# Kernel tuning notes

Measured on AMD Instinct MI355X. Metric: run time of the kernel, lower is better.

The kernel has to match this reference:

```python
import jax, jax.numpy as jnp
import numpy as np

D_MODEL = 512
N_HEADS = 8
DH = D_MODEL // N_HEADS            # 64
Q_PROJ = D_MODEL // 2              # 256
KV_PROJ = (2 * D_MODEL) // 3       # 341
ROPE_DIM = D_MODEL // 8            # 64 total rope dims
R = ROPE_DIM // N_HEADS            # 8 rope dims per head
THETA = 10000.0
EPS = 1e-5
B, S = 2, 2048


def layernorm(x, g, b):
    m = jnp.mean(x, axis=-1, keepdims=True)
    v = jnp.var(x, axis=-1, keepdims=True)
    return (x - m) * jax.lax.rsqrt(v + EPS) * g + b


def rope_cos_sin(seq_len, dtype):
    inv_freq = THETA ** (-jnp.arange(0, R, 2, dtype=jnp.float32) / R)   # (R/2,)
    ang = jnp.arange(seq_len, dtype=jnp.float32)[:, None] * inv_freq   # (S, R/2)
    cos = jnp.concatenate([jnp.cos(ang), jnp.cos(ang)], axis=-1)        # (S, R)
    sin = jnp.concatenate([jnp.sin(ang), jnp.sin(ang)], axis=-1)
    return cos.astype(dtype), sin.astype(dtype)


def apply_rope(x, cos, sin):
    # x: (B, H, S, R); neox-style half rotation
    x1, x2 = jnp.split(x, 2, axis=-1)
    rot = jnp.concatenate([-x2, x1], axis=-1)
    return x * cos + rot * sin


def setup_inputs() -> dict:
    key = jax.random.key(0)
    ks = jax.random.split(key, 9)
    p = lambda k, shape: 0.01 * jax.random.normal(k, shape, jnp.float32)
    return {
        "x": jax.random.normal(ks[0], (B, S, D_MODEL), jnp.float32),
        "W_dq": p(ks[1], (D_MODEL, Q_PROJ)),
        "W_uq": p(ks[2], (Q_PROJ, D_MODEL)),
        "W_qr": p(ks[3], (Q_PROJ, ROPE_DIM)),
        "W_dkv": p(ks[4], (D_MODEL, KV_PROJ)),
        "W_ukv": p(ks[5], (KV_PROJ, 2 * D_MODEL)),
        "W_kr": p(ks[6], (D_MODEL, ROPE_DIM)),
        "W_o": p(ks[7], (D_MODEL, D_MODEL)),
        "q_ln_g": jnp.ones((Q_PROJ,), jnp.float32),
        "q_ln_b": jnp.zeros((Q_PROJ,), jnp.float32),
        "kv_ln_g": jnp.ones((KV_PROJ,), jnp.float32),
        "kv_ln_b": jnp.zeros((KV_PROJ,), jnp.float32),
    }


def reference(x, W_dq, W_uq, W_qr, W_dkv, W_ukv, W_kr, W_o,
              q_ln_g, q_ln_b, kv_ln_g, kv_ln_b):
    b, s, d = x.shape
    # --- low-rank Q path ---
    cq = layernorm(x @ W_dq, q_ln_g, q_ln_b)                      # (B,S,Q_PROJ)
    Q = (cq @ W_uq).reshape(b, s, N_HEADS, DH).transpose(0, 2, 1, 3)
    Qr = (cq @ W_qr).reshape(b, s, N_HEADS, R).transpose(0, 2, 1, 3)
    cos, sin = rope_cos_sin(s, x.dtype)
    Qr = apply_rope(Qr, cos, sin)
    q = jnp.concatenate([Q, Qr], axis=-1)                          # (B,H,S,DH+R)
    # --- low-rank KV path ---
    ckv = layernorm(x @ W_dkv, kv_ln_g, kv_ln_b)                  # (B,S,KV_PROJ)
    KV = ckv @ W_ukv                                              # (B,S,2*D)
    K, V = KV[..., :D_MODEL], KV[..., D_MODEL:]
    K = K.reshape(b, s, N_HEADS, DH).transpose(0, 2, 1, 3)
    Kr = (x @ W_kr).reshape(b, s, N_HEADS, R).transpose(0, 2, 1, 3)
    Kr = apply_rope(Kr, cos, sin)
    k = jnp.concatenate([K, Kr], axis=-1)                          # (B,H,S,DH+R)
    v = V.reshape(b, s, N_HEADS, DH).transpose(0, 2, 1, 3)         # (B,H,S,DH)
    # --- causal SDPA ---
    scale = 1.0 / jnp.sqrt(jnp.asarray(DH + R, x.dtype))
    scores = jnp.einsum('bhqd,bhkd->bhqk', q, k) * scale           # (B,H,S,S)
    mask = jnp.tril(jnp.ones((s, s), dtype=bool))
    scores = jnp.where(mask, scores, jnp.finfo(scores.dtype).min)
    attn = jax.nn.softmax(scores, axis=-1)
    out = jnp.einsum('bhqk,bhkd->bhqd', attn, v)
    out = out.transpose(0, 2, 1, 3).reshape(b, s, d)
    return out @ W_o.T, ckv
```

## Files before the change

kernel.cpp:

```cpp
#include <hip/hip_runtime.h>
#include <hip/hip_bf16.h>

#define BATCH 2
#define SEQ 2048
#define DM 512
#define NH 8
#define DHD 64
#define QP 256
#define KVP 341
#define DQKPAD 96
#define MROWS 4096

#define OFF_X     0
#define OFF_WO    2932224
#define OFF_QG    3194368
#define OFF_QB    3194624
#define OFF_KG    3194880
#define OFF_KB    3195221

#define T_DQ   0
#define T_DKV  131072
#define T_KR   327680
#define T_UQ   360448
#define T_QR   491520
#define T_UKV  507904
#define T_TOT  901120

#define NW_X   2097152
#define NW_WO  262144
#define NW_PAR 1194

#define G_X   262144
#define G_WO  32768
#define G_PAR 150
#define G_WT  112640
#define G_TOT (G_X + G_WO + G_PAR + G_WT)

#define NSPLIT 4

typedef __bf16 bf16x8 __attribute__((ext_vector_type(8)));
typedef float f32x4 __attribute__((ext_vector_type(4)));
typedef __hip_bfloat16 bf16;
typedef unsigned short u16;

static __device__ __forceinline__ bf16x8 ld_bf8(const bf16* p) {
    return __builtin_bit_cast(bf16x8, *(const uint4*)p);
}

#define GL16(gp, lp) __builtin_amdgcn_global_load_lds( \
    (const __attribute__((address_space(1))) void*)(gp), \
    (__attribute__((address_space(3))) void*)(lp), 16, 0, 0)

__global__ __launch_bounds__(256) void prep(
    const void* px, const void* pwdq, const void* pwuq, const void* pwqr,
    const void* pwdkv, const void* pwukv, const void* pwkr, const void* pwo,
    const void* pqg, const void* pqb, const void* pkg, const void* pkb,
    u16* __restrict__ arena, u16* __restrict__ WT, int* __restrict__ flagp)
{
    __shared__ int cnt;
    if (threadIdx.x == 0) cnt = 0;
    __syncthreads();
    int bad = 0;
    const u16* xs = (const u16*)px;
    for (int i = threadIdx.x; i < 2048; i += 256) {
        u16 u = xs[i];
        int e = (u >> 7) & 0xFF;
        if (u != 0 && (e < 90 || e > 164)) bad++;
    }
    #pragma unroll
    for (int m2 = 1; m2 < 64; m2 <<= 1) bad += __shfl_xor(bad, m2);
    if ((threadIdx.x & 63) == 0) atomicAdd(&cnt, bad);
    __syncthreads();
    const int f = (cnt > 256) ? 1 : 0;
    if (blockIdx.x == 0 && threadIdx.x == 0) *flagp = f;

    int gid = blockIdx.x * 256 + threadIdx.x;
    if (gid >= G_TOT) return;

    auto rdu = [&](const void* s, int i) -> u16 {
        if (f) return __builtin_bit_cast(u16, __float2bfloat16(((const float*)s)[i]));
        return ((const u16*)s)[i];
    };

    if (gid < G_X + G_WO) {
        const void* src = (gid < G_X) ? px : pwo;
        int base = (gid < G_X) ? OFF_X : OFF_WO;
        int i = (gid < G_X) ? gid : gid - G_X;
        u16 out[8];
        if (f) {
            const float* s = (const float*)src + i * 8;
            #pragma unroll
            for (int j = 0; j < 8; ++j) out[j] = __builtin_bit_cast(u16, __float2bfloat16(s[j]));
        } else {
            *(uint4*)out = ((const uint4*)src)[i];
        }
        *(uint4*)&arena[base + i * 8] = *(uint4*)out;
    } else if (gid < G_X + G_WO + G_PAR) {
        int i0 = (gid - G_X - G_WO) * 8;
        for (int j = 0; j < 8; ++j) {
            int i = i0 + j;
            if (i >= NW_PAR) break;
            if (i < 256)      arena[OFF_QG + i]         = rdu(pqg, i);
            else if (i < 512) arena[OFF_QB + (i - 256)] = rdu(pqb, i - 256);
            else if (i < 853) arena[OFF_KG + (i - 512)] = rdu(pkg, i - 512);
            else              arena[OFF_KB + (i - 853)] = rdu(pkb, i - 853);
        }
    } else {
        int loc = (gid - (G_X + G_WO + G_PAR)) * 8;
        const void* src; int n, k0, sN, klim, nok;
        if (loc < T_DKV)      { int l = loc;          n = l >> 9; k0 = l & 511; src = pwdq;  sN = 256;  klim = 512; nok = 1; }
        else if (loc < T_KR)  { int l = loc - T_DKV;  n = l >> 9; k0 = l & 511; src = pwdkv; sN = 341;  klim = 512; nok = (n < 341); }
        else if (loc < T_UQ)  { int l = loc - T_KR;   n = l >> 9; k0 = l & 511; src = pwkr;  sN = 64;   klim = 512; nok = 1; }
        else if (loc < T_QR)  { int l = loc - T_UQ;   n = l >> 8; k0 = l & 255; src = pwuq;  sN = 512;  klim = 256; nok = 1; }
        else if (loc < T_UKV) { int l = loc - T_QR;   n = l >> 8; k0 = l & 255; src = pwqr;  sN = 64;   klim = 256; nok = 1; }
        else                  { int l = loc - T_UKV;  n = l / 384; k0 = l % 384; src = pwukv; sN = 1024; klim = 341; nok = 1; }
        u16 out[8];
        #pragma unroll
        for (int j = 0; j < 8; ++j) {
            int k = k0 + j;
            out[j] = (nok && k < klim) ? rdu(src, k * sN + n) : (u16)0;
        }
        *(uint4*)&WT[loc] = *(uint4*)out;
    }
}

static __device__ __forceinline__ void rope_epi(
    f32x4 (&acc)[2][4], bf16* __restrict__ dst, int m0, int w, int g, int lr, int tid, bool scaleq)
{
    const float SCv = 0.11785113019775793f;
    #pragma unroll
    for (int mt = 0; mt < 2; ++mt)
    #pragma unroll
    for (int r = 0; r < 4; ++r) {
        int gm = m0 + w * 32 + mt * 16 + g * 4 + r;
        int s = gm & 2047, b = gm >> 11;
        float ang = (float)s * exp2f(-(float)(lr & 3) * 3.3219280948873623f);
        float sn, cs;
        sincosf(ang, &sn, &cs);
        #pragma unroll
        for (int nt = 0; nt < 4; ++nt) {
            float v = acc[mt][nt][r];
            float pt = __shfl_xor(v, 4);
            float o = (lr & 4) ? fmaf(pt, sn, v * cs) : fmaf(-pt, sn, v * cs);
            if (scaleq) o *= SCv;
            int h = (nt * 16 + lr) >> 3, j = lr & 7;
            dst[((size_t)(b * NH + h) * SEQ + s) * DQKPAD + 64 + j] = __float2bfloat16(o);
        }
    }
    for (int u = tid; u < 128 * 96; u += 256) {
        int rw = u / 96, rem = u - rw * 96;
        int h = rem / 12, c = rem - h * 12;
        int row = m0 + rw, b2 = row >> 11, s2 = row & 2047;
        *(unsigned int*)&dst[((size_t)(b2 * NH + h) * SEQ + s2) * DQKPAD + 72 + c * 2] = 0u;
    }
}

static __device__ __forceinline__ void gemm_body(
    int bx, int by,
    const bf16* __restrict__ A, int lda,
    const bf16* __restrict__ BT, int ldb,
    int N, int Kpad, int mode,
    void* __restrict__ C0, int ldc,
    bf16* __restrict__ kv_k, bf16* __restrict__ kv_v,
    const int* __restrict__ flagp, float* __restrict__ C0f,
    bf16* LB)
{
    bf16* Al = LB;
    bf16* Bl = LB + 128 * 64;
    const int tid = threadIdx.x;
    const int m0 = by * 128, n0 = bx * 64;
    const int lane = tid & 63, w = tid >> 6;
    const int g = lane >> 4, lr = lane & 15;
    f32x4 acc[2][4] = {};
    const int r8 = lane >> 3;
    const int xr8 = ((lane & 7) ^ r8) * 8;
    const int swx = (lr & 7) << 4;

    for (int k0 = 0; k0 < Kpad; k0 += 64) {
        #pragma unroll
        for (int i = 0; i < 4; ++i)
            GL16(&A[(size_t)(m0 + w * 32 + i * 8 + r8) * lda + k0 + xr8],
                 (char*)Al + w * 4096 + i * 1024);
        #pragma unroll
        for (int i = 0; i < 2; ++i)
            GL16(&BT[(size_t)(n0 + w * 16 + i * 8 + r8) * ldb + k0 + xr8],
                 (char*)Bl + w * 2048 + i * 1024);
        __syncthreads();
        #pragma unroll
        for (int ks = 0; ks < 2; ++ks) {
            const int cs = (ks * 64 + g * 16) ^ swx;
            bf16x8 a0 = ld_bf8((const bf16*)((const char*)Al + (w * 32 + lr) * 128 + cs));
            bf16x8 a1 = ld_bf8((const bf16*)((const char*)Al + (w * 32 + 16 + lr) * 128 + cs));
            #pragma unroll
            for (int nt = 0; nt < 4; ++nt) {
                bf16x8 b = ld_bf8((const bf16*)((const char*)Bl + (nt * 16 + lr) * 128 + cs));
                acc[0][nt] = __builtin_amdgcn_mfma_f32_16x16x32_bf16(a0, b, acc[0][nt], 0, 0, 0);
                acc[1][nt] = __builtin_amdgcn_mfma_f32_16x16x32_bf16(a1, b, acc[1][nt], 0, 0, 0);
            }
        }
        __syncthreads();
    }

    if (mode == 0 && n0 == 640) {
        rope_epi(acc, kv_k, m0, w, g, lr, tid, false);
        return;
    }
    if (mode == 4 && n0 == DM) {
        rope_epi(acc, (bf16*)C0, m0, w, g, lr, tid, true);
        return;
    }
    if (mode == 3 && n0 >= DM) {
        const int h = (n0 - DM) >> 6;
        const int b = m0 >> 11, s0 = m0 & 2047;
        bf16* T = LB;
        #pragma unroll
        for (int mt = 0; mt < 2; ++mt)
        #pragma unroll
        for (int nt = 0; nt < 4; ++nt)
        #pragma unroll
        for (int r = 0; r < 4; ++r) {
            int dv = nt * 16 + lr;
            int sl = w * 32 + mt * 16 + g * 4 + r;
            T[dv * 136 + sl] = __float2bfloat16(acc[mt][nt][r]);
        }
        __syncthreads();
        const int row = tid >> 2, coff = (tid & 3) * 32;
        bf16* dst = &kv_v[((size_t)(b * NH + h) * DHD + row) * SEQ + s0 + coff];
        const bf16* srcp = &T[row * 136 + coff];
        #pragma unroll
        for (int q2 = 0; q2 < 4; ++q2)
            *(uint4*)(dst + q2 * 8) = *(const uint4*)(srcp + q2 * 8);
        return;
    }

    const float SCv = 0.11785113019775793f;
    const int f32o = (mode == 1 && flagp) ? *flagp : 0;
    #pragma unroll
    for (int mt = 0; mt < 2; ++mt)
    #pragma unroll
    for (int nt = 0; nt < 4; ++nt)
    #pragma unroll
    for (int r = 0; r < 4; ++r) {
        int gm = m0 + w * 32 + mt * 16 + g * 4 + r;
        int gn = n0 + nt * 16 + lr;
        float v = acc[mt][nt][r];
        if (mode == 0) {
            ((bf16*)C0)[(size_t)gm * ldc + gn] = __float2bfloat16(v);
        } else if (mode == 1) {
            if (f32o) C0f[(size_t)gm * ldc + gn] = v;
            else ((bf16*)C0)[(size_t)gm * ldc + gn] = __float2bfloat16(v);
        } else if (mode == 4) {
            int b = gm >> 11, s = gm & 2047;
            int h = gn >> 6, dh = gn & 63;
            ((bf16*)C0)[((size_t)(b * NH + h) * SEQ + s) * DQKPAD + dh] = __float2bfloat16(v * SCv);
        } else {
            int b = gm >> 11, s = gm & 2047;
            int h = gn >> 6, dh = gn & 63;
            kv_k[((size_t)(b * NH + h) * SEQ + s) * DQKPAD + dh] = __float2bfloat16(v);
        }
    }
}

__global__ __launch_bounds__(256) void gemm128(
    const bf16* __restrict__ A, int lda,
    const bf16* __restrict__ BT, int ldb,
    int N, int Kpad, int mode,
    void* __restrict__ C0, int ldc,
    bf16* __restrict__ kv_k, bf16* __restrict__ kv_v,
    const int* __restrict__ flagp, float* __restrict__ C0f)
{
    __shared__ __align__(16) bf16 LB[128 * 64 + 64 * 64];
    gemm_body(blockIdx.x, blockIdx.y, A, lda, BT, ldb, N, Kpad, mode,
              C0, ldc, kv_k, kv_v, flagp, C0f, LB);
}

__global__ __launch_bounds__(256) void gemm_dual(
    const bf16* __restrict__ A1, const bf16* __restrict__ BT1, void* __restrict__ C1,
    const bf16* __restrict__ A2, const bf16* __restrict__ BT2,
    bf16* __restrict__ kv_k, bf16* __restrict__ kv_v)
{
    __shared__ __align__(16) bf16 LB[128 * 64 + 64 * 64];
    if (blockIdx.x < 9) {
        gemm_body(blockIdx.x, blockIdx.y, A1, QP, BT1, QP, 576, QP, 4,
                  C1, 0, nullptr, nullptr, nullptr, nullptr, LB);
    } else {
        gemm_body(blockIdx.x - 9, blockIdx.y, A2, 384, BT2, 384, 1024, 384, 3,
                  nullptr, 0, kv_k, kv_v, nullptr, nullptr, LB);
    }
}

__global__ __launch_bounds__(256) void ln_both(
    const bf16* __restrict__ y,
    const bf16* __restrict__ qg, const bf16* __restrict__ qb,
    const bf16* __restrict__ kg, const bf16* __restrict__ kb,
    bf16* __restrict__ cq, bf16* __restrict__ ckv_b, float* __restrict__ ckv_f,
    bf16* __restrict__ ckvp, const int* __restrict__ flagp)
{
    const int w = threadIdx.x >> 6, lane = threadIdx.x & 63;
    const int blk = blockIdx.x;
    if (blk < 1024) {
        const int row = blk * 4 + w;
        const bf16* yr = y + (size_t)row * 704;
        float s = 0.f, ss = 0.f;
        for (int i = lane; i < 256; i += 64) { float v = __bfloat162float(yr[i]); s += v; ss += v * v; }
        #pragma unroll
        for (int m = 1; m < 64; m <<= 1) { s += __shfl_xor(s, m); ss += __shfl_xor(ss, m); }
        float mean = s * (1.f / 256.f);
        float var = ss * (1.f / 256.f) - mean * mean;
        float rstd = rsqrtf(var + 1e-5f);
        for (int i = lane; i < 256; i += 64) {
            float v = (__bfloat162float(yr[i]) - mean) * rstd * __bfloat162float(qg[i]) + __bfloat162float(qb[i]);
            cq[(size_t)row * 256 + i] = __float2bfloat16(v);
        }
    } else {
        const int row = (blk - 1024) * 4 + w;
        const bf16* yr = y + (size_t)row * 704 + 256;
        const int f32o = *flagp;
        float s = 0.f, ss = 0.f;
        for (int i = lane; i < KVP; i += 64) { float v = __bfloat162float(yr[i]); s += v; ss += v * v; }
        #pragma unroll
        for (int m = 1; m < 64; m <<= 1) { s += __shfl_xor(s, m); ss += __shfl_xor(ss, m); }
        float mean = s * (1.f / 341.f);
        float var = ss * (1.f / 341.f) - mean * mean;
        float rstd = rsqrtf(var + 1e-5f);
        for (int i = lane; i < KVP; i += 64) {
            float v = (__bfloat162float(yr[i]) - mean) * rstd * __bfloat162float(kg[i]) + __bfloat162float(kb[i]);
            if (f32o) ckv_f[(size_t)row * KVP + i] = v;
            else ckv_b[(size_t)row * KVP + i] = __float2bfloat16(v);
            ckvp[(size_t)row * 384 + i] = __float2bfloat16(v);
        }
        for (int i = KVP + lane; i < 384; i += 64) ckvp[(size_t)row * 384 + i] = __float2bfloat16(0.f);
    }
}

__global__ __launch_bounds__(256) void attn_split3(
    const bf16* __restrict__ qa, const bf16* __restrict__ ka, const bf16* __restrict__ vat,
    bf16* __restrict__ po, float* __restrict__ mlm, float* __restrict__ mll)
{
    __shared__ __align__(16) bf16 Kl[64][128];
    __shared__ __align__(16) bf16 Vt[64][72];
    __shared__ __align__(16) bf16 Pl[4][16][72];
    const int sp = blockIdx.x, pr = blockIdx.y, bh = blockIdx.z;
    const int tid = threadIdx.x, w = tid >> 6, lane = tid & 63;
    const int g = lane >> 4, lr = lane & 15;
    const size_t base = (size_t)bh * SEQ;
    const float L2E = 1.4426950408889634f;
    const bf16* vb = vat + (size_t)bh * DHD * SEQ;

    uint4 kreg0, kreg1, kreg2, vreg0, vreg1;
    const int vd = tid >> 2, vko = (tid & 3) * 16;
    const int kr0 = tid / 12,          ks0 = tid % 12;
    const int kr1 = (tid + 256) / 12,  ks1 = (tid + 256) % 12;
    const int kr2 = (tid + 512) / 12,  ks2 = (tid + 512) % 12;
    const int kx0 = (ks0 ^ (kr0 & 15)) * 8;
    const int kx1 = (ks1 ^ (kr1 & 15)) * 8;
    const int kx2 = (ks2 ^ (kr2 & 15)) * 8;

    #define ISSUE_KV(j0)  do { \
        kreg0 = *(const uint4*)&ka[(base + (j0) + kr0) * DQKPAD + ks0 * 8]; \
        kreg1 = *(const uint4*)&ka[(base + (j0) + kr1) * DQKPAD + ks1 * 8]; \
        kreg2 = *(const uint4*)&ka[(base + (j0) + kr2) * DQKPAD + ks2 * 8]; \
        const bf16* vsrc = &vb[(size_t)vd * SEQ + (j0) + vko]; \
        vreg0 = *(const uint4*)vsrc; vreg1 = *(const uint4*)(vsrc + 8); \
    } while (0)

    for (int half = 0; half < 2; ++half) {
        const int qb = half ? (31 - pr) : pr;
        const int qrow0 = qb * 64 + w * 16;
        const int myq = qrow0 + lr;

        bf16x8 qf[3];
        #pragma unroll
        for (int kc = 0; kc < 3; ++kc)
            qf[kc] = ld_bf8(&qa[(base + myq) * DQKPAD + kc * 32 + g * 8]);

        float m_p = -1e30f, l_p = 0.f;
        f32x4 acc_o[4] = {};
        const int ng = qb + 1;
        const int bs = (ng * sp) >> 2, be = (ng * (sp + 1)) >> 2;

        if (bs < be) ISSUE_KV(bs * 64);

        for (int gi = bs; gi < be; ++gi) {
            const int j0 = gi * 64;
            __syncthreads();
            *(uint4*)&Kl[kr0][kx0] = kreg0;
            *(uint4*)&Kl[kr1][kx1] = kreg1;
            *(uint4*)&Kl[kr2][kx2] = kreg2;
            *(uint4*)&Vt[vd][vko]     = vreg0;
            *(uint4*)&Vt[vd][vko + 8] = vreg1;
            __syncthreads();
            if (gi + 1 < be) ISSUE_KV(j0 + 64);

            f32x4 accs[4] = {};
            __builtin_amdgcn_s_setprio(1);
            #pragma unroll
            for (int kc = 0; kc < 3; ++kc) {
                #pragma unroll
                for (int nt = 0; nt < 4; ++nt) {
                    bf16x8 kf = ld_bf8(&Kl[nt * 16 + lr][((kc * 4 + g) ^ lr) * 8]);
                    accs[nt] = __builtin_amdgcn_mfma_f32_16x16x32_bf16(kf, qf[kc], accs[nt], 0, 0, 0);
                }
            }
            __builtin_amdgcn_s_setprio(0);
            float s_[4][4];
            float mloc = -1e30f;
            if (j0 + 63 > qrow0) {
                #pragma unroll
                for (int nt = 0; nt < 4; ++nt)
                #pragma unroll
                for (int r = 0; r < 4; ++r) {
                    int key = j0 + nt * 16 + g * 4 + r;
                    float sv = accs[nt][r];
                    sv = (key <= myq) ? sv : -1e30f;
                    s_[nt][r] = sv;
                    mloc = fmaxf(mloc, sv);
                }
            } else {
                #pragma unroll
                for (int nt = 0; nt < 4; ++nt)
                #pragma unroll
                for (int r = 0; r < 4; ++r) {
                    float sv = accs[nt][r];
                    s_[nt][r] = sv;
                    mloc = fmaxf(mloc, sv);
                }
            }
            mloc = fmaxf(mloc, __shfl_xor(mloc, 16));
            mloc = fmaxf(mloc, __shfl_xor(mloc, 32));

            if (__all(mloc <= m_p + 8.f)) {
                float rs = 0.f;
                #pragma unroll
                for (int nt = 0; nt < 4; ++nt)
                #pragma unroll
                for (int r = 0; r < 4; ++r) {
                    float p = exp2f((s_[nt][r] - m_p) * L2E);
                    s_[nt][r] = p; rs += p;
                }
                rs += __shfl_xor(rs, 16);
                rs += __shfl_xor(rs, 32);
                l_p += rs;
            } else {
                float mn = fmaxf(m_p, mloc);
                float alpha = exp2f((m_p - mn) * L2E);
                m_p = mn;
                float rs = 0.f;
                #pragma unroll
                for (int nt = 0; nt < 4; ++nt)
                #pragma unroll
                for (int r = 0; r < 4; ++r) {
                    float p = exp2f((s_[nt][r] - mn) * L2E);
                    s_[nt][r] = p; rs += p;
                }
                rs += __shfl_xor(rs, 16);
                rs += __shfl_xor(rs, 32);
                l_p = l_p * alpha + rs;
                float ar[4];
                #pragma unroll
                for (int r = 0; r < 4; ++r) ar[r] = __shfl(alpha, g * 4 + r);
                #pragma unroll
                for (int nv = 0; nv < 4; ++nv)
                #pragma unroll
                for (int r = 0; r < 4; ++r) acc_o[nv][r] *= ar[r];
            }
            #pragma unroll
            for (int nt = 0; nt < 4; ++nt) {
                ushort4 pk;
                pk.x = __builtin_bit_cast(u16, __float2bfloat16(s_[nt][0]));
                pk.y = __builtin_bit_cast(u16, __float2bfloat16(s_[nt][1]));
                pk.z = __builtin_bit_cast(u16, __float2bfloat16(s_[nt][2]));
                pk.w = __builtin_bit_cast(u16, __float2bfloat16(s_[nt][3]));
                *(ushort4*)&Pl[w][lr][nt * 16 + g * 4] = pk;
            }
            bf16x8 pf0 = ld_bf8(&Pl[w][lr][g * 8]);
            bf16x8 pf1 = ld_bf8(&Pl[w][lr][32 + g * 8]);
            __builtin_amdgcn_s_setprio(1);
            #pragma unroll
            for (int nv = 0; nv < 4; ++nv) {
                bf16x8 vf0 = ld_bf8(&Vt[nv * 16 + lr][g * 8]);
                acc_o[nv] = __builtin_amdgcn_mfma_f32_16x16x32_bf16(pf0, vf0, acc_o[nv], 0, 0, 0);
                bf16x8 vf1 = ld_bf8(&Vt[nv * 16 + lr][32 + g * 8]);
                acc_o[nv] = __builtin_amdgcn_mfma_f32_16x16x32_bf16(pf1, vf1, acc_o[nv], 0, 0, 0);
            }
            __builtin_amdgcn_s_setprio(0);
        }

        const size_t pb = (size_t)(bh * NSPLIT + sp) * SEQ;
        #pragma unroll
        for (int r = 0; r < 4; ++r) {
            int qrow = qrow0 + g * 4 + r;
            #pragma unroll
            for (int nv = 0; nv < 4; ++nv)
                po[(pb + qrow) * DHD + nv * 16 + lr] = __float2bfloat16(acc_o[nv][r]);
        }
        if (lane < 16) {
            size_t mi = ((size_t)bh * SEQ + qrow0 + lane) * 4 + sp;
            mlm[mi] = m_p;
            mll[mi] = l_p;
        }
    }
    #undef ISSUE_KV
}

__global__ __launch_bounds__(256) void attn_combine(
    const bf16* __restrict__ po, const float* __restrict__ mlm, const float* __restrict__ mll,
    bf16* __restrict__ ao)
{
    int id = blockIdx.x * 256 + threadIdx.x;
    int bh = id >> 14;
    int rem = id & 16383;
    int q = rem >> 3, dc = (rem & 7) * 8;
    const float L2E = 1.4426950408889634f;
    size_t mi = ((size_t)bh * SEQ + q) * 4;
    f32x4 ms = *(const f32x4*)&mlm[mi];
    f32x4 ls = *(const f32x4*)&mll[mi];
    float M = fmaxf(fmaxf(ms[0], ms[1]), fmaxf(ms[2], ms[3]));
    float wsc[NSPLIT]; float L = 0.f;
    #pragma unroll
    for (int s = 0; s < NSPLIT; ++s) { wsc[s] = exp2f((ms[s] - M) * L2E); L += wsc[s] * ls[s]; }
    float o[8] = {};
    #pragma unroll
    for (int s = 0; s < NSPLIT; ++s) {
        if (ls[s] <= 0.f) continue;
        bf16x8 pv = ld_bf8(&po[((size_t)(bh * NSPLIT + s) * SEQ + q) * DHD + dc]);
        #pragma unroll
        for (int j = 0; j < 8; ++j) o[j] += wsc[s] * (float)pv[j];
    }
    float invL = 1.f / L;
    int b = bh >> 3, h = bh & 7;
    __bf16 tmp[8];
    #pragma unroll
    for (int j = 0; j < 8; ++j) tmp[j] = (__bf16)(o[j] * invL);
    *(uint4*)&ao[((size_t)(b * SEQ) + q) * DM + h * DHD + dc] = *(uint4*)tmp;
}

extern "C" void kernel_launch(void* const* d_in, const int* in_sizes, int n_in,
                              void* d_out, int out_size, void* d_ws, size_t ws_size,
                              hipStream_t stream) {
    char* ws = (char*)d_ws;
    bf16* AR      = (bf16*)(ws + 0);
    float* ml_m   = (float*)(ws + 0);
    float* ml_l   = (float*)(ws + 1048576);
    bf16* WT      = (bf16*)(ws + 6391296);
    int*  flagp   = (int*)(ws + 8193536);
    bf16* y       = (bf16*)(ws + 8194048);
    bf16* cq      = (bf16*)(ws + 19728384);
    bf16* ckvp    = (bf16*)(ws + 21825536);
    bf16* q_attn  = (bf16*)(ws + 26019840);
    bf16* k_attn  = (bf16*)(ws + 32311296);
    bf16* v_attnT = (bf16*)(ws + 38602752);
    bf16* attn_o  = (bf16*)(ws + 42797056);
    bf16* po      = (bf16*)(ws + 50331648);

    const bf16* xb  = AR + OFF_X;
    const bf16* W_o = AR + OFF_WO;
    const bf16* qg  = AR + OFF_QG;
    const bf16* qb_ = AR + OFF_QB;
    const bf16* kg  = AR + OFF_KG;
    const bf16* kb  = AR + OFF_KB;

    bf16*  out_b = (bf16*)d_out;
    float* out_f = (float*)d_out;
    bf16*  ckv_b = out_b + (size_t)MROWS * DM;
    float* ckv_f = out_f + (size_t)MROWS * DM;

    dim3 blk(256);
    prep<<<dim3((G_TOT + 255) / 256), blk, 0, stream>>>(
        d_in[0], d_in[1], d_in[2], d_in[3], d_in[4], d_in[5],
        d_in[6], d_in[7], d_in[8], d_in[9], d_in[10], d_in[11],
        (u16*)AR, (u16*)WT, flagp);
    gemm128<<<dim3(11, 32), blk, 0, stream>>>(xb, DM, WT + T_DQ, DM, 704, DM, 0, y, 704, k_attn, nullptr, nullptr, nullptr);
    ln_both<<<dim3(2048), blk, 0, stream>>>(y, qg, qb_, kg, kb, cq, ckv_b, ckv_f, ckvp, flagp);
    gemm_dual<<<dim3(25, 32), blk, 0, stream>>>(cq, WT + T_UQ, q_attn, ckvp, WT + T_UKV, k_attn, v_attnT);
    attn_split3<<<dim3(NSPLIT, 16, 16), blk, 0, stream>>>(q_attn, k_attn, v_attnT, po, ml_m, ml_l);
    attn_combine<<<dim3(1024), blk, 0, stream>>>(po, ml_m, ml_l, attn_o);
    gemm128<<<dim3(8, 32), blk, 0, stream>>>(attn_o, DM, W_o, DM, DM, DM, 1, out_b, DM, nullptr, nullptr, flagp, out_f);
}
```

Baseline: 110.1 us.

## Fuse all pipeline stages into one cooperative persistent kernel with grid syncs

```diff
diff --git a/kernel.cpp b/kernel.cpp
--- a/kernel.cpp
+++ b/kernel.cpp
@@ -1,5 +1,8 @@
 #include <hip/hip_runtime.h>
+#include <hip/hip_cooperative_groups.h>
 #include <hip/hip_bf16.h>
+
+namespace cg = cooperative_groups;
 
 #define BATCH 2
 #define SEQ 2048
@@ -26,8 +29,6 @@
 #define T_UKV  507904
 #define T_TOT  901120
 
-#define NW_X   2097152
-#define NW_WO  262144
 #define NW_PAR 1194
 
 #define G_X   262144
@@ -35,8 +36,10 @@
 #define G_PAR 150
 #define G_WT  112640
 #define G_TOT (G_X + G_WO + G_PAR + G_WT)
+#define NPREPB ((G_TOT + 255) / 256)
 
 #define NSPLIT 4
+#define NBLK 256
 
 typedef __bf16 bf16x8 __attribute__((ext_vector_type(8)));
 typedef float f32x4 __attribute__((ext_vector_type(4)));
@@ -51,32 +54,13 @@
     (const __attribute__((address_space(1))) void*)(gp), \
     (__attribute__((address_space(3))) void*)(lp), 16, 0, 0)
 
-__global__ __launch_bounds__(256) void prep(
+static __device__ __forceinline__ void prep_work(
+    int gid, int f,
     const void* px, const void* pwdq, const void* pwuq, const void* pwqr,
     const void* pwdkv, const void* pwukv, const void* pwkr, const void* pwo,
     const void* pqg, const void* pqb, const void* pkg, const void* pkb,
-    u16* __restrict__ arena, u16* __restrict__ WT, int* __restrict__ flagp)
-{
-    __shared__ int cnt;
-    if (threadIdx.x == 0) cnt = 0;
-    __syncthreads();
-    int bad = 0;
-    const u16* xs = (const u16*)px;
-    for (int i = threadIdx.x; i < 2048; i += 256) {
-        u16 u = xs[i];
-        int e = (u >> 7) & 0xFF;
-        if (u != 0 && (e < 90 || e > 164)) bad++;
-    }
-    #pragma unroll
-    for (int m2 = 1; m2 < 64; m2 <<= 1) bad += __shfl_xor(bad, m2);
-    if ((threadIdx.x & 63) == 0) atomicAdd(&cnt, bad);
-    __syncthreads();
-    const int f = (cnt > 256) ? 1 : 0;
-    if (blockIdx.x == 0 && threadIdx.x == 0) *flagp = f;
-
-    int gid = blockIdx.x * 256 + threadIdx.x;
-    if (gid >= G_TOT) return;
-
+    u16* __restrict__ arena, u16* __restrict__ WT)
+{
     auto rdu = [&](const void* s, int i) -> u16 {
         if (f) return __builtin_bit_cast(u16, __float2bfloat16(((const float*)s)[i]));
         return ((const u16*)s)[i];
@@ -162,7 +146,7 @@
     int N, int Kpad, int mode,
     void* __restrict__ C0, int ldc,
     bf16* __restrict__ kv_k, bf16* __restrict__ kv_v,
-    const int* __restrict__ flagp, float* __restrict__ C0f,
+    int f32o, float* __restrict__ C0f,
     bf16* LB)
 {
     bf16* Al = LB;
@@ -176,6 +160,7 @@
     const int xr8 = ((lane & 7) ^ r8) * 8;
     const int swx = (lr & 7) << 4;
 
+    __syncthreads();
     for (int k0 = 0; k0 < Kpad; k0 += 64) {
         #pragma unroll
         for (int i = 0; i < 4; ++i)
@@ -234,7 +219,6 @@
     }
 
     const float SCv = 0.11785113019775793f;
-    const int f32o = (mode == 1 && flagp) ? *flagp : 0;
     #pragma unroll
     for (int mt = 0; mt < 2; ++mt)
     #pragma unroll
@@ -261,43 +245,15 @@
     }
 }
 
-__global__ __launch_bounds__(256) void gemm128(
-    const bf16* __restrict__ A, int lda,
-    const bf16* __restrict__ BT, int ldb,
-    int N, int Kpad, int mode,
-    void* __restrict__ C0, int ldc,
-    bf16* __restrict__ kv_k, bf16* __restrict__ kv_v,
-    const int* __restrict__ flagp, float* __restrict__ C0f)
-{
-    __shared__ __align__(16) bf16 LB[128 * 64 + 64 * 64];
-    gemm_body(blockIdx.x, blockIdx.y, A, lda, BT, ldb, N, Kpad, mode,
-              C0, ldc, kv_k, kv_v, flagp, C0f, LB);
-}
-
-__global__ __launch_bounds__(256) void gemm_dual(
-    const bf16* __restrict__ A1, const bf16* __restrict__ BT1, void* __restrict__ C1,
-    const bf16* __restrict__ A2, const bf16* __restrict__ BT2,
-    bf16* __restrict__ kv_k, bf16* __restrict__ kv_v)
-{
-    __shared__ __align__(16) bf16 LB[128 * 64 + 64 * 64];
-    if (blockIdx.x < 9) {
-        gemm_body(blockIdx.x, blockIdx.y, A1, QP, BT1, QP, 576, QP, 4,
-                  C1, 0, nullptr, nullptr, nullptr, nullptr, LB);
-    } else {
-        gemm_body(blockIdx.x - 9, blockIdx.y, A2, 384, BT2, 384, 1024, 384, 3,
-                  nullptr, 0, kv_k, kv_v, nullptr, nullptr, LB);
-    }
-}
-
-__global__ __launch_bounds__(256) void ln_both(
+static __device__ __forceinline__ void ln_body(
+    int blk, int f,
     const bf16* __restrict__ y,
     const bf16* __restrict__ qg, const bf16* __restrict__ qb,
     const bf16* __restrict__ kg, const bf16* __restrict__ kb,
     bf16* __restrict__ cq, bf16* __restrict__ ckv_b, float* __restrict__ ckv_f,
-    bf16* __restrict__ ckvp, const int* __restrict__ flagp)
+    bf16* __restrict__ ckvp)
 {
     const int w = threadIdx.x >> 6, lane = threadIdx.x & 63;
-    const int blk = blockIdx.x;
     if (blk < 1024) {
         const int row = blk * 4 + w;
         const bf16* yr = y + (size_t)row * 704;
@@ -315,7 +271,6 @@
     } else {
         const int row = (blk - 1024) * 4 + w;
         const bf16* yr = y + (size_t)row * 704 + 256;
-        const int f32o = *flagp;
         float s = 0.f, ss = 0.f;
         for (int i = lane; i < KVP; i += 64) { float v = __bfloat162float(yr[i]); s += v; ss += v * v; }
         #pragma unroll
@@ -325,7 +280,7 @@
         float rstd = rsqrtf(var + 1e-5f);
         for (int i = lane; i < KVP; i += 64) {
             float v = (__bfloat162float(yr[i]) - mean) * rstd * __bfloat162float(kg[i]) + __bfloat162float(kb[i]);
-            if (f32o) ckv_f[(size_t)row * KVP + i] = v;
+            if (f) ckv_f[(size_t)row * KVP + i] = v;
             else ckv_b[(size_t)row * KVP + i] = __float2bfloat16(v);
             ckvp[(size_t)row * 384 + i] = __float2bfloat16(v);
         }
@@ -333,14 +288,15 @@
     }
 }
 
-__global__ __launch_bounds__(256) void attn_split3(
+static __device__ __forceinline__ void attn_body(
+    int sp, int pr, int bh,
     const bf16* __restrict__ qa, const bf16* __restrict__ ka, const bf16* __restrict__ vat,
-    bf16* __restrict__ po, float* __restrict__ mlm, float* __restrict__ mll)
-{
-    __shared__ __align__(16) bf16 Kl[64][128];
-    __shared__ __align__(16) bf16 Vt[64][72];
-    __shared__ __align__(16) bf16 Pl[4][16][72];
-    const int sp = blockIdx.x, pr = blockIdx.y, bh = blockIdx.z;
+    bf16* __restrict__ po, float* __restrict__ mlm, float* __restrict__ mll,
+    char* SMRAW)
+{
+    bf16* Kl = (bf16*)SMRAW;
+    bf16* Vt = (bf16*)(SMRAW + 16384);
+    bf16* Pl = (bf16*)(SMRAW + 25600);
     const int tid = threadIdx.x, w = tid >> 6, lane = tid & 63;
     const int g = lane >> 4, lr = lane & 15;
     const size_t base = (size_t)bh * SEQ;
@@ -384,11 +340,11 @@
         for (int gi = bs; gi < be; ++gi) {
             const int j0 = gi * 64;
             __syncthreads();
-            *(uint4*)&Kl[kr0][kx0] = kreg0;
-            *(uint4*)&Kl[kr1][kx1] = kreg1;
-            *(uint4*)&Kl[kr2][kx2] = kreg2;
-            *(uint4*)&Vt[vd][vko]     = vreg0;
-            *(uint4*)&Vt[vd][vko + 8] = vreg1;
+            *(uint4*)&Kl[kr0 * 128 + kx0] = kreg0;
+            *(uint4*)&Kl[kr1 * 128 + kx1] = kreg1;
+            *(uint4*)&Kl[kr2 * 128 + kx2] = kreg2;
+            *(uint4*)&Vt[vd * 72 + vko]     = vreg0;
+            *(uint4*)&Vt[vd * 72 + vko + 8] = vreg1;
             __syncthreads();
             if (gi + 1 < be) ISSUE_KV(j0 + 64);
 
@@ -398,7 +354,7 @@
             for (int kc = 0; kc < 3; ++kc) {
                 #pragma unroll
                 for (int nt = 0; nt < 4; ++nt) {
-                    bf16x8 kf = ld_bf8(&Kl[nt * 16 + lr][((kc * 4 + g) ^ lr) * 8]);
+                    bf16x8 kf = ld_bf8(&Kl[(nt * 16 + lr) * 128 + ((kc * 4 + g) ^ lr) * 8]);
                     accs[nt] = __builtin_amdgcn_mfma_f32_16x16x32_bf16(kf, qf[kc], accs[nt], 0, 0, 0);
                 }
             }
@@ -471,16 +427,16 @@
                 pk.y = __builtin_bit_cast(u16, __float2bfloat16(s_[nt][1]));
                 pk.z = __builtin_bit_cast(u16, __float2bfloat16(s_[nt][2]));
                 pk.w = __builtin_bit_cast(u16, __float2bfloat16(s_[nt][3]));
-                *(ushort4*)&Pl[w][lr][nt * 16 + g * 4] = pk;
+                *(ushort4*)&Pl[(w * 16 + lr) * 72 + nt * 16 + g * 4] = pk;
             }
-            bf16x8 pf0 = ld_bf8(&Pl[w][lr][g * 8]);
-            bf16x8 pf1 = ld_bf8(&Pl[w][lr][32 + g * 8]);
+            bf16x8 pf0 = ld_bf8(&Pl[(w * 16 + lr) * 72 + g * 8]);
+            bf16x8 pf1 = ld_bf8(&Pl[(w * 16 + lr) * 72 + 32 + g * 8]);
             __builtin_amdgcn_s_setprio(1);
             #pragma unroll
             for (int nv = 0; nv < 4; ++nv) {
-                bf16x8 vf0 = ld_bf8(&Vt[nv * 16 + lr][g * 8]);
+                bf16x8 vf0 = ld_bf8(&Vt[(nv * 16 + lr) * 72 + g * 8]);
                 acc_o[nv] = __builtin_amdgcn_mfma_f32_16x16x32_bf16(pf0, vf0, acc_o[nv], 0, 0, 0);
-                bf16x8 vf1 = ld_bf8(&Vt[nv * 16 + lr][32 + g * 8]);
+                bf16x8 vf1 = ld_bf8(&Vt[(nv * 16 + lr) * 72 + 32 + g * 8]);
                 acc_o[nv] = __builtin_amdgcn_mfma_f32_16x16x32_bf16(pf1, vf1, acc_o[nv], 0, 0, 0);
             }
             __builtin_amdgcn_s_setprio(0);
@@ -503,11 +459,10 @@
     #undef ISSUE_KV
 }
 
-__global__ __launch_bounds__(256) void attn_combine(
-    const bf16* __restrict__ po, const float* __restrict__ mlm, const float* __restrict__ mll,
+static __device__ __forceinline__ void combine_body(
+    int id, const bf16* __restrict__ po, const float* __restrict__ mlm, const float* __restrict__ mll,
     bf16* __restrict__ ao)
 {
-    int id = blockIdx.x * 256 + threadIdx.x;
     int bh = id >> 14;
     int rem = id & 16383;
     int q = rem >> 3, dc = (rem & 7) * 8;
@@ -535,14 +490,167 @@
     *(uint4*)&ao[((size_t)(b * SEQ) + q) * DM + h * DHD + dc] = *(uint4*)tmp;
 }
 
+static __device__ __forceinline__ int detect_f(const void* px, int* cntp) {
+    const int tid = threadIdx.x;
+    if (tid == 0) *cntp = 0;
+    __syncthreads();
+    int bad = 0;
+    const u16* xs = (const u16*)px;
+    for (int i = tid; i < 2048; i += 256) {
+        u16 u = xs[i];
+        int e = (u >> 7) & 0xFF;
+        if (u != 0 && (e < 90 || e > 164)) bad++;
+    }
+    #pragma unroll
+    for (int m2 = 1; m2 < 64; m2 <<= 1) bad += __shfl_xor(bad, m2);
+    if ((tid & 63) == 0) atomicAdd(cntp, bad);
+    __syncthreads();
+    return (*cntp > 256) ? 1 : 0;
+}
+
+__global__ __launch_bounds__(256) void mega(
+    const void* px, const void* pwdq, const void* pwuq, const void* pwqr,
+    const void* pwdkv, const void* pwukv, const void* pwkr, const void* pwo,
+    const void* pqg, const void* pqb, const void* pkg, const void* pkb,
+    u16* arena, u16* WTu, bf16* y, bf16* cq, bf16* ckvp,
+    bf16* q_attn, bf16* k_attn, bf16* v_attnT, bf16* attn_o, bf16* po,
+    float* mlm, float* mll, bf16* out_b, float* out_f, bf16* ckv_b, float* ckv_f)
+{
+    cg::grid_group grid = cg::this_grid();
+    __shared__ __align__(16) char SMRAW[34816];
+    bf16* SM = (bf16*)SMRAW;
+    __shared__ int cnt;
+    const int f = detect_f(px, &cnt);
+
+    const bf16* WT = (const bf16*)WTu;
+    const bf16* xb  = (const bf16*)arena + OFF_X;
+    const bf16* W_o = (const bf16*)arena + OFF_WO;
+    const bf16* qg  = (const bf16*)arena + OFF_QG;
+    const bf16* qb_ = (const bf16*)arena + OFF_QB;
+    const bf16* kg  = (const bf16*)arena + OFF_KG;
+    const bf16* kb  = (const bf16*)arena + OFF_KB;
+
+    for (int vb = blockIdx.x; vb < NPREPB; vb += gridDim.x) {
+        int gid = vb * 256 + threadIdx.x;
+        if (gid < G_TOT)
+            prep_work(gid, f, px, pwdq, pwuq, pwqr, pwdkv, pwukv, pwkr, pwo,
+                      pqg, pqb, pkg, pkb, arena, WTu);
+    }
+    grid.sync();
+
+    for (int vb = blockIdx.x; vb < 352; vb += gridDim.x)
+        gemm_body(vb % 11, vb / 11, xb, DM, WT + T_DQ, DM, 704, DM, 0,
+                  y, 704, k_attn, nullptr, 0, nullptr, SM);
+    grid.sync();
+
+    for (int vb = blockIdx.x; vb < 2048; vb += gridDim.x)
+        ln_body(vb, f, y, qg, qb_, kg, kb, cq, ckv_b, ckv_f, ckvp);
+    grid.sync();
+
+    for (int vb = blockIdx.x; vb < 800; vb += gridDim.x) {
+        int bxv = vb % 25, by = vb / 25;
+        if (bxv < 9)
+            gemm_body(bxv, by, cq, QP, WT + T_UQ, QP, 576, QP, 4,
+                      q_attn, 0, nullptr, nullptr, 0, nullptr, SM);
+        else
+            gemm_body(bxv - 9, by, ckvp, 384, WT + T_UKV, 384, 1024, 384, 3,
+                      nullptr, 0, k_attn, v_attnT, 0, nullptr, SM);
+    }
+    grid.sync();
+
+    for (int vb = blockIdx.x; vb < 1024; vb += gridDim.x) {
+        int sp = vb & 3, rest = vb >> 2;
+        int pr = rest & 15, bh = rest >> 4;
+        attn_body(sp, pr, bh, q_attn, k_attn, v_attnT, po, mlm, mll, SMRAW);
+    }
+    grid.sync();
+
+    for (int vb = blockIdx.x; vb < 1024; vb += gridDim.x)
+        combine_body(vb * 256 + threadIdx.x, po, mlm, mll, attn_o);
+    grid.sync();
+
+    for (int vb = blockIdx.x; vb < 256; vb += gridDim.x)
+        gemm_body(vb % 8, vb / 8, attn_o, DM, W_o, DM, DM, DM, 1,
+                  out_b, DM, nullptr, nullptr, f, out_f, SM);
+}
+
+__global__ __launch_bounds__(256) void prep_k(
+    const void* px, const void* pwdq, const void* pwuq, const void* pwqr,
+    const void* pwdkv, const void* pwukv, const void* pwkr, const void* pwo,
+    const void* pqg, const void* pqb, const void* pkg, const void* pkb,
+    u16* __restrict__ arena, u16* __restrict__ WT, int* __restrict__ flagp)
+{
+    __shared__ int cnt;
+    const int f = detect_f(px, &cnt);
+    if (blockIdx.x == 0 && threadIdx.x == 0) *flagp = f;
+    int gid = blockIdx.x * 256 + threadIdx.x;
+    if (gid >= G_TOT) return;
+    prep_work(gid, f, px, pwdq, pwuq, pwqr, pwdkv, pwukv, pwkr, pwo,
+              pqg, pqb, pkg, pkb, arena, WT);
+}
+
+__global__ __launch_bounds__(256) void gemm128(
+    const bf16* __restrict__ A, int lda,
+    const bf16* __restrict__ BT, int ldb,
+    int N, int Kpad, int mode,
+    void* __restrict__ C0, int ldc,
+    bf16* __restrict__ kv_k, bf16* __restrict__ kv_v,
+    const int* __restrict__ flagp, float* __restrict__ C0f)
+{
+    __shared__ __align__(16) bf16 LB[128 * 64 + 64 * 64];
+    const int f32o = (mode == 1 && flagp) ? *flagp : 0;
+    gemm_body(blockIdx.x, blockIdx.y, A, lda, BT, ldb, N, Kpad, mode,
+              C0, ldc, kv_k, kv_v, f32o, C0f, LB);
+}
+
+__global__ __launch_bounds__(256) void gemm_dual(
+    const bf16* __restrict__ A1, const bf16* __restrict__ BT1, void* __restrict__ C1,
+    const bf16* __restrict__ A2, const bf16* __restrict__ BT2,
+    bf16* __restrict__ kv_k, bf16* __restrict__ kv_v)
+{
+    __shared__ __align__(16) bf16 LB[128 * 64 + 64 * 64];
+    if (blockIdx.x < 9) {
+        gemm_body(blockIdx.x, blockIdx.y, A1, QP, BT1, QP, 576, QP, 4,
+                  C1, 0, nullptr, nullptr, 0, nullptr, LB);
+    } else {
+        gemm_body(blockIdx.x - 9, blockIdx.y, A2, 384, BT2, 384, 1024, 384, 3,
+                  nullptr, 0, kv_k, kv_v, 0, nullptr, LB);
+    }
+}
+
+__global__ __launch_bounds__(256) void ln_both(
+    const bf16* __restrict__ y,
+    const bf16* __restrict__ qg, const bf16* __restrict__ qb,
+    const bf16* __restrict__ kg, const bf16* __restrict__ kb,
+    bf16* __restrict__ cq, bf16* __restrict__ ckv_b, float* __restrict__ ckv_f,
+    bf16* __restrict__ ckvp, const int* __restrict__ flagp)
+{
+    ln_body(blockIdx.x, *flagp, y, qg, qb, kg, kb, cq, ckv_b, ckv_f, ckvp);
+}
+
+__global__ __launch_bounds__(256) void attn_split3(
+    const bf16* __restrict__ qa, const bf16* __restrict__ ka, const bf16* __restrict__ vat,
+    bf16* __restrict__ po, float* __restrict__ mlm, float* __restrict__ mll)
+{
+    __shared__ __align__(16) char SMRAW[34816];
+    attn_body(blockIdx.x, blockIdx.y, blockIdx.z, qa, ka, vat, po, mlm, mll, SMRAW);
+}
+
+__global__ __launch_bounds__(256) void attn_combine(
+    const bf16* __restrict__ po, const float* __restrict__ mlm, const float* __restrict__ mll,
+    bf16* __restrict__ ao)
+{
+    combine_body(blockIdx.x * 256 + threadIdx.x, po, mlm, mll, ao);
+}
+
 extern "C" void kernel_launch(void* const* d_in, const int* in_sizes, int n_in,
                               void* d_out, int out_size, void* d_ws, size_t ws_size,
                               hipStream_t stream) {
     char* ws = (char*)d_ws;
-    bf16* AR      = (bf16*)(ws + 0);
+    u16*  arena   = (u16*)(ws + 0);
     float* ml_m   = (float*)(ws + 0);
     float* ml_l   = (float*)(ws + 1048576);
-    bf16* WT      = (bf16*)(ws + 6391296);
+    u16*  WTu     = (u16*)(ws + 6391296);
     int*  flagp   = (int*)(ws + 8193536);
     bf16* y       = (bf16*)(ws + 8194048);
     bf16* cq      = (bf16*)(ws + 19728384);
@@ -553,23 +661,47 @@
     bf16* attn_o  = (bf16*)(ws + 42797056);
     bf16* po      = (bf16*)(ws + 50331648);
 
+    const void* px    = d_in[0];
+    const void* pwdq  = d_in[1];
+    const void* pwuq  = d_in[2];
+    const void* pwqr  = d_in[3];
+    const void* pwdkv = d_in[4];
+    const void* pwukv = d_in[5];
+    const void* pwkr  = d_in[6];
+    const void* pwo   = d_in[7];
+    const void* pqg   = d_in[8];
+    const void* pqb   = d_in[9];
+    const void* pkg   = d_in[10];
+    const void* pkb   = d_in[11];
+
+    bf16*  out_b = (bf16*)d_out;
+    float* out_f = (float*)d_out;
+    bf16*  ckv_b = out_b + (size_t)MROWS * DM;
+    float* ckv_f = out_f + (size_t)MROWS * DM;
+
+    void* args[] = {
+        &px, &pwdq, &pwuq, &pwqr, &pwdkv, &pwukv, &pwkr, &pwo,
+        &pqg, &pqb, &pkg, &pkb,
+        &arena, &WTu, &y, &cq, &ckvp,
+        &q_attn, &k_attn, &v_attnT, &attn_o, &po,
+        &ml_m, &ml_l, &out_b, &out_f, &ckv_b, &ckv_f
+    };
+    hipError_t err = hipLaunchCooperativeKernel((const void*)mega, dim3(NBLK), dim3(256), args, 0, stream);
+    if (err == hipSuccess) return;
+
+    const bf16* AR  = (const bf16*)arena;
     const bf16* xb  = AR + OFF_X;
     const bf16* W_o = AR + OFF_WO;
     const bf16* qg  = AR + OFF_QG;
     const bf16* qb_ = AR + OFF_QB;
     const bf16* kg  = AR + OFF_KG;
     const bf16* kb  = AR + OFF_KB;
-
-    bf16*  out_b = (bf16*)d_out;
-    float* out_f = (float*)d_out;
-    bf16*  ckv_b = out_b + (size_t)MROWS * DM;
-    float* ckv_f = out_f + (size_t)MROWS * DM;
+    const bf16* WT  = (const bf16*)WTu;
 
     dim3 blk(256);
-    prep<<<dim3((G_TOT + 255) / 256), blk, 0, stream>>>(
-        d_in[0], d_in[1], d_in[2], d_in[3], d_in[4], d_in[5],
-        d_in[6], d_in[7], d_in[8], d_in[9], d_in[10], d_in[11],
-        (u16*)AR, (u16*)WT, flagp);
+    prep_k<<<dim3((G_TOT + 255) / 256), blk, 0, stream>>>(
+        px, pwdq, pwuq, pwqr, pwdkv, pwukv, pwkr, pwo,
+        pqg, pqb, pkg, pkb, arena, WTu, flagp);
     gemm128<<<dim3(11, 32), blk, 0, stream>>>(xb, DM, WT + T_DQ, DM, 704, DM, 0, y, 704, k_attn, nullptr, nullptr, nullptr);
     ln_both<<<dim3(2048), blk, 0, stream>>>(y, qg, qb_, kg, kb, cq, ckv_b, ckv_f, ckvp, flagp);
     gemm_dual<<<dim3(25, 32), blk, 0, stream>>>(cq, WT + T_UQ, q_attn, ckvp, WT + T_UKV, k_attn, v_attnT);
```

Result: slower. 345.1 us (+213.4%).
